# Kernel optimization log

Hardware: AMD Instinct MI355X
Metric: run time of the kernel (lower is better)

The kernel has to match this reference:

```python
import jax, jax.numpy as jnp
import numpy as np

N, E, D = 100000, 1600000, 128

def _sage_mean(x, src, dst, W_self, W_neigh, b, n_nodes):
    # mean over in-neighbors: sum messages by dst, divide by in-degree
    msg_sum = jax.ops.segment_sum(x[src], dst, num_segments=n_nodes)
    deg = jax.ops.segment_sum(jnp.ones((src.shape[0],), x.dtype), dst, num_segments=n_nodes)
    h_neigh = msg_sum / jnp.maximum(deg, 1.0)[:, None]
    # DGL SAGEConv (mean): fc_self(h) + fc_neigh(h_neigh) + bias
    return x @ W_self + h_neigh @ W_neigh + b

def setup_inputs() -> dict:
    key = jax.random.key(0)
    ks = jax.random.split(key, 9)
    s = 1.0 / np.sqrt(D)
    return {
        "x": jax.random.normal(ks[0], (N, D), jnp.float32),
        "src": jax.random.randint(ks[1], (E,), 0, N, jnp.int32),
        "dst": jax.random.randint(ks[2], (E,), 0, N, jnp.int32),
        "W_self1": jax.random.uniform(ks[3], (D, D), jnp.float32, -s, s),
        "W_neigh1": jax.random.uniform(ks[4], (D, D), jnp.float32, -s, s),
        "b1": jnp.zeros((D,), jnp.float32),
        "W_self2": jax.random.uniform(ks[5], (D, D), jnp.float32, -s, s),
        "W_neigh2": jax.random.uniform(ks[6], (D, D), jnp.float32, -s, s),
        "b2": jnp.zeros((D,), jnp.float32),
    }

def reference(x, src, dst, W_self1, W_neigh1, b1, W_self2, W_neigh2, b2):
    n = x.shape[0]
    h = jax.nn.relu(_sage_mean(x, src, dst, W_self1, W_neigh1, b1, n))
    h = jax.nn.relu(_sage_mean(h, src, dst, W_self2, W_neigh2, b2, n))
    return h
```

## Files before the change

### kernel.cpp

```cpp
#include <hip/hip_runtime.h>

#define DF 128

typedef __bf16 bf16x8_t __attribute__((ext_vector_type(8)));
typedef float f32x4_t __attribute__((ext_vector_type(4)));
typedef unsigned short ushort_t;
typedef ushort_t ushort8_t __attribute__((ext_vector_type(8)));

static __device__ __forceinline__ ushort_t f2bf(float f) {
    union { float f; unsigned int u; } v; v.f = f;
    unsigned int r = v.u + 0x7fffu + ((v.u >> 16) & 1u);
    return (ushort_t)(r >> 16);
}
static __device__ __forceinline__ float bflo(unsigned int v) {
    union { unsigned int u; float f; } c; c.u = v << 16; return c.f;
}
static __device__ __forceinline__ float bfhi(unsigned int v) {
    union { unsigned int u; float f; } c; c.u = v & 0xffff0000u; return c.f;
}


__global__ __launch_bounds__(256) void k1_coarse_hist(
    const int* __restrict__ dst, int* __restrict__ C,
    int E, int CH, int NCH, int NBKT) {
    __shared__ int lcnt[512];
    const int c = blockIdx.x;
    for (int b = threadIdx.x; b < NBKT; b += 256) lcnt[b] = 0;
    __syncthreads();
    const int base = c * CH, lim = min(base + CH, E);
    for (int i = base + threadIdx.x; i < lim; i += 256)
        atomicAdd(&lcnt[dst[i] >> 8], 1);
    __syncthreads();
    for (int b = threadIdx.x; b < NBKT; b += 256) C[b * NCH + c] = lcnt[b];
}

__global__ __launch_bounds__(512) void k2a_row_scan(
    int* __restrict__ C, int* __restrict__ rowtot, int NCH) {
    __shared__ int sd[512];
    const int b = blockIdx.x, t = threadIdx.x;
    int v = (t < NCH) ? C[b * NCH + t] : 0;
    sd[t] = v; __syncthreads();
    for (int off = 1; off < 512; off <<= 1) {
        int u = (t >= off) ? sd[t - off] : 0;
        __syncthreads();
        sd[t] += u;
        __syncthreads();
    }
    if (t < NCH) C[b * NCH + t] = sd[t] - v;
    if (t == 511) rowtot[b] = sd[511];
}

__global__ __launch_bounds__(512) void k2b_base_scan(
    const int* __restrict__ rowtot, int* __restrict__ rowbase,
    int* __restrict__ rowptr, int NBKT, int N, int E) {
    __shared__ int sd[512];
    const int t = threadIdx.x;
    int v = (t < NBKT) ? rowtot[t] : 0;
    sd[t] = v; __syncthreads();
    for (int off = 1; off < 512; off <<= 1) {
        int u = (t >= off) ? sd[t - off] : 0;
        __syncthreads();
        sd[t] += u;
        __syncthreads();
    }
    if (t < NBKT) rowbase[t] = sd[t] - v;
    if (t == 0) { rowbase[NBKT] = E; rowptr[N] = E; }
}

__global__ __launch_bounds__(256) void k3_bin_scatter(
    const int* __restrict__ src, const int* __restrict__ dst,
    const int* __restrict__ C, const int* __restrict__ rowbase,
    unsigned int* __restrict__ inter, int E, int CH, int NCH, int NBKT) {
    __shared__ int cur[512];
    const int c = blockIdx.x;
    for (int b = threadIdx.x; b < NBKT; b += 256)
        cur[b] = rowbase[b] + C[b * NCH + c];
    __syncthreads();
    const int base = c * CH, lim = min(base + CH, E);
    for (int i = base + threadIdx.x; i < lim; i += 256) {
        int d = dst[i];
        int s = src[i];
        int pos = atomicAdd(&cur[d >> 8], 1);
        inter[pos] = ((unsigned int)(d & 255) << 24) | (unsigned int)s;
    }
}

#define K4CAP 6144
__global__ __launch_bounds__(256) void k4_fine_scatter(
    const unsigned int* __restrict__ inter, const int* __restrict__ rowbase,
    int* __restrict__ edge_src, int* __restrict__ rowptr, int N) {
    __shared__ unsigned int stage[K4CAP];
    __shared__ unsigned int outv[K4CAP];
    __shared__ int lcnt[256], lofs[256], lrun[256];
    const int b = blockIdx.x, t = threadIdx.x;
    const int base = rowbase[b], count = rowbase[b + 1] - base;
    const int n0 = b << 8;
    const int nn = min(256, N - n0);

    lcnt[t] = 0; lrun[t] = 0;
    __syncthreads();

    if (count <= K4CAP) {
        for (int i = t; i < count; i += 256) {
            unsigned int v = inter[base + i];
            stage[i] = v;
            atomicAdd(&lcnt[v >> 24], 1);
        }
        __syncthreads();
        int cv = lcnt[t];
        lofs[t] = cv; __syncthreads();
        for (int off = 1; off < 256; off <<= 1) {
            int u = (t >= off) ? lofs[t - off] : 0;
            __syncthreads();
            lofs[t] += u;
            __syncthreads();
        }
        lofs[t] -= cv;
        if (t < nn) rowptr[n0 + t] = base + lofs[t];
        __syncthreads();
        for (int i = t; i < count; i += 256) {
            unsigned int v = stage[i];
            int dl = v >> 24;
            int p = lofs[dl] + atomicAdd(&lrun[dl], 1);
            outv[p] = v & 0xFFFFFFu;
        }
        __syncthreads();
        for (int i = t; i < count; i += 256) edge_src[base + i] = (int)outv[i];
    } else {
        for (int i = t; i < count; i += 256)
            atomicAdd(&lcnt[inter[base + i] >> 24], 1);
        __syncthreads();
        int cv = lcnt[t];
        lofs[t] = cv; __syncthreads();
        for (int off = 1; off < 256; off <<= 1) {
            int u = (t >= off) ? lofs[t - off] : 0;
            __syncthreads();
            lofs[t] += u;
            __syncthreads();
        }
        lofs[t] -= cv;
        if (t < nn) rowptr[n0 + t] = base + lofs[t];
        __syncthreads();
        for (int i = t; i < count; i += 256) {
            unsigned int v = inter[base + i];
            int dl = v >> 24;
            int p = atomicAdd(&lrun[dl], 1);
            edge_src[base + lofs[dl] + p] = (int)(v & 0xFFFFFFu);
        }
    }
}

__global__ __launch_bounds__(256) void conv_bf16_kernel(const float* __restrict__ in,
                                                        ushort_t* __restrict__ out, int n8) {
    int i = blockIdx.x * blockDim.x + threadIdx.x;
    if (i >= n8) return;
    float4 a = ((const float4*)in)[(size_t)i * 2];
    float4 b = ((const float4*)in)[(size_t)i * 2 + 1];
    ushort8_t o;
    o[0] = f2bf(a.x); o[1] = f2bf(a.y); o[2] = f2bf(a.z); o[3] = f2bf(a.w);
    o[4] = f2bf(b.x); o[5] = f2bf(b.y); o[6] = f2bf(b.z); o[7] = f2bf(b.w);
    ((ushort8_t*)out)[i] = o;
}

__global__ void transpose_w_kernel(const float* __restrict__ W0, const float* __restrict__ W1,
                                   const float* __restrict__ W2, const float* __restrict__ W3,
                                   ushort_t* __restrict__ out) {
    int m = blockIdx.x >> 6;
    const float* W = (m == 0) ? W0 : (m == 1) ? W1 : (m == 2) ? W2 : W3;
    int idx = (blockIdx.x & 63) * 256 + threadIdx.x;
    int k = idx >> 7, n = idx & 127;
    out[m * 16384 + n * 128 + k] = f2bf(W[idx]);
}

__global__ __launch_bounds__(256, 4) void aggregate_bf16_kernel(
    const ushort_t* __restrict__ Xb, const int* __restrict__ rowptr,
    const int* __restrict__ edge_src, ushort_t* __restrict__ out, int N) {
    int node = (int)((blockIdx.x * 256u + threadIdx.x) >> 6);
    int lane = threadIdx.x & 63;
    if (node >= N) return;
    const int g = lane >> 4;
    const int s = lane & 15;
    int beg = rowptr[node], end = rowptr[node + 1];
    int deg = end - beg;
    float acc[8] = {0.f, 0.f, 0.f, 0.f, 0.f, 0.f, 0.f, 0.f};
    for (int b0 = 0; b0 < deg; b0 += 64) {
        int nb = min(64, deg - b0);
        int idx = (lane < nb) ? edge_src[beg + b0 + lane] : 0;
        int nfull = nb >> 4;
        for (int it = 0; it < nfull; ++it) {
            int j = it * 16 + g * 4;
            int s0 = __shfl(idx, j, 64);
            int s1 = __shfl(idx, j + 1, 64);
            int s2 = __shfl(idx, j + 2, 64);
            int s3 = __shfl(idx, j + 3, 64);
            uint4 v0 = *(const uint4*)(Xb + (size_t)s0 * DF + s * 8);
            uint4 v1 = *(const uint4*)(Xb + (size_t)s1 * DF + s * 8);
            uint4 v2 = *(const uint4*)(Xb + (size_t)s2 * DF + s * 8);
            uint4 v3 = *(const uint4*)(Xb + (size_t)s3 * DF + s * 8);
            acc[0] += (bflo(v0.x) + bflo(v1.x)) + (bflo(v2.x) + bflo(v3.x));
            acc[1] += (bfhi(v0.x) + bfhi(v1.x)) + (bfhi(v2.x) + bfhi(v3.x));
            acc[2] += (bflo(v0.y) + bflo(v1.y)) + (bflo(v2.y) + bflo(v3.y));
            acc[3] += (bfhi(v0.y) + bfhi(v1.y)) + (bfhi(v2.y) + bfhi(v3.y));
            acc[4] += (bflo(v0.z) + bflo(v1.z)) + (bflo(v2.z) + bflo(v3.z));
            acc[5] += (bfhi(v0.z) + bfhi(v1.z)) + (bfhi(v2.z) + bfhi(v3.z));
            acc[6] += (bflo(v0.w) + bflo(v1.w)) + (bflo(v2.w) + bflo(v3.w));
            acc[7] += (bfhi(v0.w) + bfhi(v1.w)) + (bfhi(v2.w) + bfhi(v3.w));
        }
        if (nb & 15) {
            int j = nfull * 16 + g * 4;
            int j0 = j, j1 = j + 1, j2 = j + 2, j3 = j + 3;
            int s0 = __shfl(idx, (j0 < nb) ? j0 : 0, 64);
            int s1 = __shfl(idx, (j1 < nb) ? j1 : 0, 64);
            int s2 = __shfl(idx, (j2 < nb) ? j2 : 0, 64);
            int s3 = __shfl(idx, (j3 < nb) ? j3 : 0, 64);
            uint4 z = make_uint4(0, 0, 0, 0);
            uint4 v0 = z, v1 = z, v2 = z, v3 = z;
            if (j0 < nb) v0 = *(const uint4*)(Xb + (size_t)s0 * DF + s * 8);
            if (j1 < nb) v1 = *(const uint4*)(Xb + (size_t)s1 * DF + s * 8);
            if (j2 < nb) v2 = *(const uint4*)(Xb + (size_t)s2 * DF + s * 8);
            if (j3 < nb) v3 = *(const uint4*)(Xb + (size_t)s3 * DF + s * 8);
            acc[0] += (bflo(v0.x) + bflo(v1.x)) + (bflo(v2.x) + bflo(v3.x));
            acc[1] += (bfhi(v0.x) + bfhi(v1.x)) + (bfhi(v2.x) + bfhi(v3.x));
            acc[2] += (bflo(v0.y) + bflo(v1.y)) + (bflo(v2.y) + bflo(v3.y));
            acc[3] += (bfhi(v0.y) + bfhi(v1.y)) + (bfhi(v2.y) + bfhi(v3.y));
            acc[4] += (bflo(v0.z) + bflo(v1.z)) + (bflo(v2.z) + bflo(v3.z));
            acc[5] += (bfhi(v0.z) + bfhi(v1.z)) + (bfhi(v2.z) + bfhi(v3.z));
            acc[6] += (bflo(v0.w) + bflo(v1.w)) + (bflo(v2.w) + bflo(v3.w));
            acc[7] += (bfhi(v0.w) + bfhi(v1.w)) + (bfhi(v2.w) + bfhi(v3.w));
        }
    }
#pragma unroll
    for (int i = 0; i < 8; ++i) {
        acc[i] += __shfl_xor(acc[i], 16, 64);
        acc[i] += __shfl_xor(acc[i], 32, 64);
    }
    if (g == 0) {
        float inv = 1.0f / fmaxf((float)deg, 1.0f);
        ushort8_t o;
#pragma unroll
        for (int i = 0; i < 8; ++i) o[i] = f2bf(acc[i] * inv);
        *(ushort8_t*)(out + (size_t)node * DF + s * 8) = o;
    }
}

template <int BF16OUT>
__global__ __launch_bounds__(256, 2) void sage_mfma_kernel(
    const ushort_t* Xb, const ushort_t* __restrict__ Ab,
    const ushort_t* __restrict__ Wts, const ushort_t* __restrict__ Wtn,
    const float* __restrict__ bias, void* outv, int M) {
    __shared__ ushort_t sW[32768];

    const int lane = threadIdx.x & 63;
    const int w = threadIdx.x >> 6;
    const int l15 = lane & 15;
    const int g = lane >> 4;
    const int m0 = blockIdx.x * 128 + w * 32;

    int r0 = m0 + l15;      if (r0 >= M) r0 = M - 1;
    int r1 = m0 + 16 + l15; if (r1 >= M) r1 = M - 1;

    for (int u = threadIdx.x; u < 4096; u += 256) {
        int row = u >> 4;
        int kb  = (u & 15) << 4;
        int swz = kb ^ ((row & 7) << 4);
        const ushort_t* gp = (row < 128)
            ? (Wts + ((size_t)row << 7) + (kb >> 1))
            : (Wtn + ((size_t)(row - 128) << 7) + (kb >> 1));
        *(ushort8_t*)((char*)sW + row * 256 + swz) = *(const ushort8_t*)gp;
    }

    bf16x8_t a[2][2][4];
#pragma unroll
    for (int mat = 0; mat < 2; ++mat) {
        const ushort_t* As = mat ? Ab : Xb;
#pragma unroll
        for (int ks = 0; ks < 4; ++ks) {
            const int ko = ks * 32 + g * 8;
            a[mat][0][ks] = *(const bf16x8_t*)(As + (size_t)r0 * DF + ko);
            a[mat][1][ks] = *(const bf16x8_t*)(As + (size_t)r1 * DF + ko);
        }
    }

    __syncthreads();

    f32x4_t acc[2][8];
#pragma unroll
    for (int rf = 0; rf < 2; ++rf)
#pragma unroll
        for (int c = 0; c < 8; ++c) acc[rf][c] = (f32x4_t){0.f, 0.f, 0.f, 0.f};

#pragma unroll
    for (int mat = 0; mat < 2; ++mat) {
#pragma unroll
        for (int ks = 0; ks < 4; ++ks) {
            const int kb = ks * 64 + g * 16;
#pragma unroll
            for (int c = 0; c < 8; ++c) {
                int brow = mat * 128 + c * 16 + l15;
                bf16x8_t b = *(const bf16x8_t*)((const char*)sW + brow * 256 +
                                                (kb ^ ((brow & 7) << 4)));
                acc[0][c] = __builtin_amdgcn_mfma_f32_16x16x32_bf16(a[mat][0][ks], b, acc[0][c], 0, 0, 0);
                acc[1][c] = __builtin_amdgcn_mfma_f32_16x16x32_bf16(a[mat][1][ks], b, acc[1][c], 0, 0, 0);
            }
        }
    }

    if (m0 + 32 <= M) {
#pragma unroll
        for (int c = 0; c < 8; ++c) {
            int col = c * 16 + l15;
            float bv = bias[col];
#pragma unroll
            for (int rf = 0; rf < 2; ++rf)
#pragma unroll
                for (int j = 0; j < 4; ++j) {
                    int row = m0 + rf * 16 + g * 4 + j;
                    float v = fmaxf(acc[rf][c][j] + bv, 0.f);
                    if (BF16OUT) ((ushort_t*)outv)[(size_t)row * DF + col] = f2bf(v);
                    else         ((float*)outv)[(size_t)row * DF + col] = v;
                }
        }
    } else {
#pragma unroll
        for (int c = 0; c < 8; ++c) {
            int col = c * 16 + l15;
            float bv = bias[col];
#pragma unroll
            for (int rf = 0; rf < 2; ++rf)
#pragma unroll
                for (int j = 0; j < 4; ++j) {
                    int row = m0 + rf * 16 + g * 4 + j;
                    if (row < M) {
                        float v = fmaxf(acc[rf][c][j] + bv, 0.f);
                        if (BF16OUT) ((ushort_t*)outv)[(size_t)row * DF + col] = f2bf(v);
                        else         ((float*)outv)[(size_t)row * DF + col] = v;
                    }
                }
        }
    }
}

extern "C" void kernel_launch(void* const* d_in, const int* in_sizes, int n_in,
                              void* d_out, int out_size, void* d_ws, size_t ws_size,
                              hipStream_t stream) {
    const int N = in_sizes[0] / DF;
    const int E = in_sizes[1];

    const float* x   = (const float*)d_in[0];
    const int*   src = (const int*)d_in[1];
    const int*   dst = (const int*)d_in[2];
    const float* Ws1 = (const float*)d_in[3];
    const float* Wn1 = (const float*)d_in[4];
    const float* b1  = (const float*)d_in[5];
    const float* Ws2 = (const float*)d_in[6];
    const float* Wn2 = (const float*)d_in[7];
    const float* b2  = (const float*)d_in[8];
    float* out = (float*)d_out;

    const int NBKT = (N + 255) >> 8;
    int CH = 4096;
    int NCH = (E + CH - 1) / CH;
    while (NCH > 512) { CH <<= 1; NCH = (E + CH - 1) / CH; }

    int* rowptr   = (int*)d_ws;
    int* rowbase  = rowptr + ((N + 1 + 63) & ~63);
    int* rowtot   = rowbase + ((NBKT + 1 + 63) & ~63);
    int* C        = rowtot + ((NBKT + 63) & ~63);
    ushort_t* Wt  = (ushort_t*)(C + ((NBKT * NCH + 63) & ~63));
    int* edge_src = (int*)(Wt + 65536);
    ushort_t* Xb  = (ushort_t*)(edge_src + ((E + 63) & ~63));
    ushort_t* Ab  = Xb + (size_t)N * DF;
    unsigned int* inter = (unsigned int*)Ab;

    conv_bf16_kernel<<<(N * DF / 8 + 255) / 256, 256, 0, stream>>>(x, Xb, N * DF / 8);
    k1_coarse_hist<<<NCH, 256, 0, stream>>>(dst, C, E, CH, NCH, NBKT);
    k2a_row_scan<<<NBKT, 512, 0, stream>>>(C, rowtot, NCH);
    k2b_base_scan<<<1, 512, 0, stream>>>(rowtot, rowbase, rowptr, NBKT, N, E);
    k3_bin_scatter<<<NCH, 256, 0, stream>>>(src, dst, C, rowbase, inter, E, CH, NCH, NBKT);
    k4_fine_scatter<<<NBKT, 256, 0, stream>>>(inter, rowbase, edge_src, rowptr, N);
    transpose_w_kernel<<<256, 256, 0, stream>>>(Ws1, Wn1, Ws2, Wn2, Wt);

    const int aggGrid  = (N + 3) / 4;
    const int gemmGrid = (N + 127) / 128;

    aggregate_bf16_kernel<<<aggGrid, 256, 0, stream>>>(Xb, rowptr, edge_src, Ab, N);
    sage_mfma_kernel<1><<<gemmGrid, 256, 0, stream>>>(Xb, Ab, Wt, Wt + 16384, b1, (void*)Xb, N);
    aggregate_bf16_kernel<<<aggGrid, 256, 0, stream>>>(Xb, rowptr, edge_src, Ab, N);
    sage_mfma_kernel<0><<<gemmGrid, 256, 0, stream>>>(Xb, Ab, Wt + 32768, Wt + 49152, b2, (void*)out, N);
}
```

Measured before the change: 217.4 us.

## Gather neighbor features from fp8 copies instead of bf16 in aggregation

```diff
diff --git a/kernel.cpp b/kernel.cpp
--- a/kernel.cpp
+++ b/kernel.cpp
@@ -4,6 +4,7 @@
 
 typedef __bf16 bf16x8_t __attribute__((ext_vector_type(8)));
 typedef float f32x4_t __attribute__((ext_vector_type(4)));
+typedef float f32x2_t __attribute__((ext_vector_type(2)));
 typedef unsigned short ushort_t;
 typedef ushort_t ushort8_t __attribute__((ext_vector_type(8)));
 
@@ -12,13 +13,9 @@
     unsigned int r = v.u + 0x7fffu + ((v.u >> 16) & 1u);
     return (ushort_t)(r >> 16);
 }
-static __device__ __forceinline__ float bflo(unsigned int v) {
-    union { unsigned int u; float f; } c; c.u = v << 16; return c.f;
-}
-static __device__ __forceinline__ float bfhi(unsigned int v) {
-    union { unsigned int u; float f; } c; c.u = v & 0xffff0000u; return c.f;
-}
-
+static __device__ __forceinline__ float bf2f(ushort_t v) {
+    union { unsigned int u; float f; } c; c.u = ((unsigned int)v) << 16; return c.f;
+}
 
 __global__ __launch_bounds__(256) void k1_coarse_hist(
     const int* __restrict__ dst, int* __restrict__ C,
@@ -150,8 +147,9 @@
     }
 }
 
-__global__ __launch_bounds__(256) void conv_bf16_kernel(const float* __restrict__ in,
-                                                        ushort_t* __restrict__ out, int n8) {
+__global__ __launch_bounds__(256) void conv_dual_kernel(
+    const float* __restrict__ in, ushort_t* __restrict__ outb,
+    unsigned char* __restrict__ out8, int n8) {
     int i = blockIdx.x * blockDim.x + threadIdx.x;
     if (i >= n8) return;
     float4 a = ((const float4*)in)[(size_t)i * 2];
@@ -159,7 +157,24 @@
     ushort8_t o;
     o[0] = f2bf(a.x); o[1] = f2bf(a.y); o[2] = f2bf(a.z); o[3] = f2bf(a.w);
     o[4] = f2bf(b.x); o[5] = f2bf(b.y); o[6] = f2bf(b.z); o[7] = f2bf(b.w);
-    ((ushort8_t*)out)[i] = o;
+    ((ushort8_t*)outb)[i] = o;
+    int lo = __builtin_amdgcn_cvt_pk_fp8_f32(a.x, a.y, 0, false);
+    lo     = __builtin_amdgcn_cvt_pk_fp8_f32(a.z, a.w, lo, true);
+    int hi = __builtin_amdgcn_cvt_pk_fp8_f32(b.x, b.y, 0, false);
+    hi     = __builtin_amdgcn_cvt_pk_fp8_f32(b.z, b.w, hi, true);
+    ((uint2*)out8)[i] = make_uint2((unsigned int)lo, (unsigned int)hi);
+}
+
+__global__ __launch_bounds__(256) void conv_b2f8_kernel(
+    const ushort_t* __restrict__ in, unsigned char* __restrict__ out8, int n8) {
+    int i = blockIdx.x * blockDim.x + threadIdx.x;
+    if (i >= n8) return;
+    ushort8_t v = ((const ushort8_t*)in)[i];
+    int lo = __builtin_amdgcn_cvt_pk_fp8_f32(bf2f(v[0]), bf2f(v[1]), 0, false);
+    lo     = __builtin_amdgcn_cvt_pk_fp8_f32(bf2f(v[2]), bf2f(v[3]), lo, true);
+    int hi = __builtin_amdgcn_cvt_pk_fp8_f32(bf2f(v[4]), bf2f(v[5]), 0, false);
+    hi     = __builtin_amdgcn_cvt_pk_fp8_f32(bf2f(v[6]), bf2f(v[7]), hi, true);
+    ((uint2*)out8)[i] = make_uint2((unsigned int)lo, (unsigned int)hi);
 }
 
 __global__ void transpose_w_kernel(const float* __restrict__ W0, const float* __restrict__ W1,
@@ -172,8 +187,8 @@
     out[m * 16384 + n * 128 + k] = f2bf(W[idx]);
 }
 
-__global__ __launch_bounds__(256, 4) void aggregate_bf16_kernel(
-    const ushort_t* __restrict__ Xb, const int* __restrict__ rowptr,
+__global__ __launch_bounds__(256, 4) void aggregate_fp8_kernel(
+    const unsigned char* __restrict__ Xf8, const int* __restrict__ rowptr,
     const int* __restrict__ edge_src, ushort_t* __restrict__ out, int N) {
     int node = (int)((blockIdx.x * 256u + threadIdx.x) >> 6);
     int lane = threadIdx.x & 63;
@@ -182,7 +197,7 @@
     const int s = lane & 15;
     int beg = rowptr[node], end = rowptr[node + 1];
     int deg = end - beg;
-    float acc[8] = {0.f, 0.f, 0.f, 0.f, 0.f, 0.f, 0.f, 0.f};
+    f32x2_t ac0 = {0.f, 0.f}, ac1 = {0.f, 0.f}, ac2 = {0.f, 0.f}, ac3 = {0.f, 0.f};
     for (int b0 = 0; b0 < deg; b0 += 64) {
         int nb = min(64, deg - b0);
         int idx = (lane < nb) ? edge_src[beg + b0 + lane] : 0;
@@ -193,18 +208,26 @@
             int s1 = __shfl(idx, j + 1, 64);
             int s2 = __shfl(idx, j + 2, 64);
             int s3 = __shfl(idx, j + 3, 64);
-            uint4 v0 = *(const uint4*)(Xb + (size_t)s0 * DF + s * 8);
-            uint4 v1 = *(const uint4*)(Xb + (size_t)s1 * DF + s * 8);
-            uint4 v2 = *(const uint4*)(Xb + (size_t)s2 * DF + s * 8);
-            uint4 v3 = *(const uint4*)(Xb + (size_t)s3 * DF + s * 8);
-            acc[0] += (bflo(v0.x) + bflo(v1.x)) + (bflo(v2.x) + bflo(v3.x));
-            acc[1] += (bfhi(v0.x) + bfhi(v1.x)) + (bfhi(v2.x) + bfhi(v3.x));
-            acc[2] += (bflo(v0.y) + bflo(v1.y)) + (bflo(v2.y) + bflo(v3.y));
-            acc[3] += (bfhi(v0.y) + bfhi(v1.y)) + (bfhi(v2.y) + bfhi(v3.y));
-            acc[4] += (bflo(v0.z) + bflo(v1.z)) + (bflo(v2.z) + bflo(v3.z));
-            acc[5] += (bfhi(v0.z) + bfhi(v1.z)) + (bfhi(v2.z) + bfhi(v3.z));
-            acc[6] += (bflo(v0.w) + bflo(v1.w)) + (bflo(v2.w) + bflo(v3.w));
-            acc[7] += (bfhi(v0.w) + bfhi(v1.w)) + (bfhi(v2.w) + bfhi(v3.w));
+            uint2 v0 = *(const uint2*)(Xf8 + (size_t)s0 * DF + s * 8);
+            uint2 v1 = *(const uint2*)(Xf8 + (size_t)s1 * DF + s * 8);
+            uint2 v2 = *(const uint2*)(Xf8 + (size_t)s2 * DF + s * 8);
+            uint2 v3 = *(const uint2*)(Xf8 + (size_t)s3 * DF + s * 8);
+            ac0 += __builtin_amdgcn_cvt_pk_f32_fp8((int)v0.x, false);
+            ac1 += __builtin_amdgcn_cvt_pk_f32_fp8((int)v0.x, true);
+            ac2 += __builtin_amdgcn_cvt_pk_f32_fp8((int)v0.y, false);
+            ac3 += __builtin_amdgcn_cvt_pk_f32_fp8((int)v0.y, true);
+            ac0 += __builtin_amdgcn_cvt_pk_f32_fp8((int)v1.x, false);
+            ac1 += __builtin_amdgcn_cvt_pk_f32_fp8((int)v1.x, true);
+            ac2 += __builtin_amdgcn_cvt_pk_f32_fp8((int)v1.y, false);
+            ac3 += __builtin_amdgcn_cvt_pk_f32_fp8((int)v1.y, true);
+            ac0 += __builtin_amdgcn_cvt_pk_f32_fp8((int)v2.x, false);
+            ac1 += __builtin_amdgcn_cvt_pk_f32_fp8((int)v2.x, true);
+            ac2 += __builtin_amdgcn_cvt_pk_f32_fp8((int)v2.y, false);
+            ac3 += __builtin_amdgcn_cvt_pk_f32_fp8((int)v2.y, true);
+            ac0 += __builtin_amdgcn_cvt_pk_f32_fp8((int)v3.x, false);
+            ac1 += __builtin_amdgcn_cvt_pk_f32_fp8((int)v3.x, true);
+            ac2 += __builtin_amdgcn_cvt_pk_f32_fp8((int)v3.y, false);
+            ac3 += __builtin_amdgcn_cvt_pk_f32_fp8((int)v3.y, true);
         }
         if (nb & 15) {
             int j = nfull * 16 + g * 4;
@@ -213,32 +236,41 @@
             int s1 = __shfl(idx, (j1 < nb) ? j1 : 0, 64);
             int s2 = __shfl(idx, (j2 < nb) ? j2 : 0, 64);
             int s3 = __shfl(idx, (j3 < nb) ? j3 : 0, 64);
-            uint4 z = make_uint4(0, 0, 0, 0);
-            uint4 v0 = z, v1 = z, v2 = z, v3 = z;
-            if (j0 < nb) v0 = *(const uint4*)(Xb + (size_t)s0 * DF + s * 8);
-            if (j1 < nb) v1 = *(const uint4*)(Xb + (size_t)s1 * DF + s * 8);
-            if (j2 < nb) v2 = *(const uint4*)(Xb + (size_t)s2 * DF + s * 8);
-            if (j3 < nb) v3 = *(const uint4*)(Xb + (size_t)s3 * DF + s * 8);
-            acc[0] += (bflo(v0.x) + bflo(v1.x)) + (bflo(v2.x) + bflo(v3.x));
-            acc[1] += (bfhi(v0.x) + bfhi(v1.x)) + (bfhi(v2.x) + bfhi(v3.x));
-            acc[2] += (bflo(v0.y) + bflo(v1.y)) + (bflo(v2.y) + bflo(v3.y));
-            acc[3] += (bfhi(v0.y) + bfhi(v1.y)) + (bfhi(v2.y) + bfhi(v3.y));
-            acc[4] += (bflo(v0.z) + bflo(v1.z)) + (bflo(v2.z) + bflo(v3.z));
-            acc[5] += (bfhi(v0.z) + bfhi(v1.z)) + (bfhi(v2.z) + bfhi(v3.z));
-            acc[6] += (bflo(v0.w) + bflo(v1.w)) + (bflo(v2.w) + bflo(v3.w));
-            acc[7] += (bfhi(v0.w) + bfhi(v1.w)) + (bfhi(v2.w) + bfhi(v3.w));
-        }
-    }
+            uint2 z = make_uint2(0, 0);
+            uint2 v0 = z, v1 = z, v2 = z, v3 = z;
+            if (j0 < nb) v0 = *(const uint2*)(Xf8 + (size_t)s0 * DF + s * 8);
+            if (j1 < nb) v1 = *(const uint2*)(Xf8 + (size_t)s1 * DF + s * 8);
+            if (j2 < nb) v2 = *(const uint2*)(Xf8 + (size_t)s2 * DF + s * 8);
+            if (j3 < nb) v3 = *(const uint2*)(Xf8 + (size_t)s3 * DF + s * 8);
+            ac0 += __builtin_amdgcn_cvt_pk_f32_fp8((int)v0.x, false);
+            ac1 += __builtin_amdgcn_cvt_pk_f32_fp8((int)v0.x, true);
+            ac2 += __builtin_amdgcn_cvt_pk_f32_fp8((int)v0.y, false);
+            ac3 += __builtin_amdgcn_cvt_pk_f32_fp8((int)v0.y, true);
+            ac0 += __builtin_amdgcn_cvt_pk_f32_fp8((int)v1.x, false);
+            ac1 += __builtin_amdgcn_cvt_pk_f32_fp8((int)v1.x, true);
+            ac2 += __builtin_amdgcn_cvt_pk_f32_fp8((int)v1.y, false);
+            ac3 += __builtin_amdgcn_cvt_pk_f32_fp8((int)v1.y, true);
+            ac0 += __builtin_amdgcn_cvt_pk_f32_fp8((int)v2.x, false);
+            ac1 += __builtin_amdgcn_cvt_pk_f32_fp8((int)v2.x, true);
+            ac2 += __builtin_amdgcn_cvt_pk_f32_fp8((int)v2.y, false);
+            ac3 += __builtin_amdgcn_cvt_pk_f32_fp8((int)v2.y, true);
+            ac0 += __builtin_amdgcn_cvt_pk_f32_fp8((int)v3.x, false);
+            ac1 += __builtin_amdgcn_cvt_pk_f32_fp8((int)v3.x, true);
+            ac2 += __builtin_amdgcn_cvt_pk_f32_fp8((int)v3.y, false);
+            ac3 += __builtin_amdgcn_cvt_pk_f32_fp8((int)v3.y, true);
+        }
+    }
+    float r[8] = {ac0[0], ac0[1], ac1[0], ac1[1], ac2[0], ac2[1], ac3[0], ac3[1]};
 #pragma unroll
     for (int i = 0; i < 8; ++i) {
-        acc[i] += __shfl_xor(acc[i], 16, 64);
-        acc[i] += __shfl_xor(acc[i], 32, 64);
+        r[i] += __shfl_xor(r[i], 16, 64);
+        r[i] += __shfl_xor(r[i], 32, 64);
     }
     if (g == 0) {
         float inv = 1.0f / fmaxf((float)deg, 1.0f);
         ushort8_t o;
 #pragma unroll
-        for (int i = 0; i < 8; ++i) o[i] = f2bf(acc[i] * inv);
+        for (int i = 0; i < 8; ++i) o[i] = f2bf(r[i] * inv);
         *(ushort8_t*)(out + (size_t)node * DF + s * 8) = o;
     }
 }
@@ -372,7 +404,10 @@
     ushort_t* Ab  = Xb + (size_t)N * DF;
     unsigned int* inter = (unsigned int*)Ab;
 
-    conv_bf16_kernel<<<(N * DF / 8 + 255) / 256, 256, 0, stream>>>(x, Xb, N * DF / 8);
+    unsigned char* Xf8  = (unsigned char*)d_out;
+    unsigned char* H1f8 = Xf8 + (size_t)N * DF;
+
+    conv_dual_kernel<<<(N * DF / 8 + 255) / 256, 256, 0, stream>>>(x, Xb, Xf8, N * DF / 8);
     k1_coarse_hist<<<NCH, 256, 0, stream>>>(dst, C, E, CH, NCH, NBKT);
     k2a_row_scan<<<NBKT, 512, 0, stream>>>(C, rowtot, NCH);
     k2b_base_scan<<<1, 512, 0, stream>>>(rowtot, rowbase, rowptr, NBKT, N, E);
@@ -383,8 +418,9 @@
     const int aggGrid  = (N + 3) / 4;
     const int gemmGrid = (N + 127) / 128;
 
-    aggregate_bf16_kernel<<<aggGrid, 256, 0, stream>>>(Xb, rowptr, edge_src, Ab, N);
+    aggregate_fp8_kernel<<<aggGrid, 256, 0, stream>>>(Xf8, rowptr, edge_src, Ab, N);
     sage_mfma_kernel<1><<<gemmGrid, 256, 0, stream>>>(Xb, Ab, Wt, Wt + 16384, b1, (void*)Xb, N);
-    aggregate_bf16_kernel<<<aggGrid, 256, 0, stream>>>(Xb, rowptr, edge_src, Ab, N);
+    conv_b2f8_kernel<<<(N * DF / 8 + 255) / 256, 256, 0, stream>>>(Xb, H1f8, N * DF / 8);
+    aggregate_fp8_kernel<<<aggGrid, 256, 0, stream>>>(H1f8, rowptr, edge_src, Ab, N);
     sage_mfma_kernel<0><<<gemmGrid, 256, 0, stream>>>(Xb, Ab, Wt + 32768, Wt + 49152, b2, (void*)out, N);
 }
```

Measured after the change: 196.7 us. 1.11x faster.
